# Performance work log

Hardware: AMD Instinct MI355X
Metric: run time of the kernel (lower is better)

The kernel has to match this reference:

```python
import jax, jax.numpy as jnp
import numpy as np

G1 = 8      # channel groups
G2 = 16     # spatial blocks per side
C1, C2 = 128, 64
H1 = W1 = 128
H2 = W2 = 256
BS1 = H1 // G2   # 8  -> 64 elems per x1 block
BS2 = H2 // G2   # 16 -> 256 elems per x2 block
BN_EPS = 1e-5


def setup_inputs() -> dict:
    key = jax.random.key(0)
    ks = jax.random.split(key, 16)
    B = 4
    c1g, c2g = C1 // G1, C2 // G1          # 16, 8
    inp = {
        "x1": jax.random.normal(ks[0], (B, C1, H1, W1), jnp.float32),
        "x2": jax.random.normal(ks[1], (B, C2, H2, W2), jnp.float32),
        # Conv1: conv1d k=1, C1//G1 -> C1//2//G1  (16 -> 8)
        "w_c1": jax.random.normal(ks[2], (c1g // 2, c1g), jnp.float32) * 0.1,
        "b_c1": jnp.zeros((c1g // 2,), jnp.float32),
        # Conv2: conv1d k=1, C2//G1 -> C2//G1  (8 -> 8)
        "w_c2": jax.random.normal(ks[3], (c2g, c2g), jnp.float32) * 0.1,
        "b_c2": jnp.zeros((c2g,), jnp.float32),
        # conv1 / conv2: 1x1 conv2d to 1 channel
        "w_p1": jax.random.normal(ks[4], (C1,), jnp.float32) * 0.1,
        "b_p1": jnp.zeros((), jnp.float32),
        "w_p2": jax.random.normal(ks[5], (C2,), jnp.float32) * 0.1,
        "b_p2": jnp.zeros((), jnp.float32),
        # SpatialAttention linear: 64 -> 256 (torch weight layout [out, in])
        "w_lin": jax.random.normal(ks[6], (BS2 * BS2, BS1 * BS1), jnp.float32) * 0.1,
        "b_lin": jnp.zeros((BS2 * BS2,), jnp.float32),
        # convbnrelu: 1x1 conv C2->C2 + BN (eval mode, running stats mean=0 var=1)
        "w_f": jax.random.normal(ks[7], (C2, C2), jnp.float32) * 0.05,
        "b_f": jnp.zeros((C2,), jnp.float32),
        "bn_gamma": jnp.ones((C2,), jnp.float32),
        "bn_beta": jnp.zeros((C2,), jnp.float32),
    }
    return inp


def reference(x1, x2, w_c1, b_c1, w_c2, b_c2, w_p1, b_p1, w_p2, b_p2,
              w_lin, b_lin, w_f, b_f, bn_gamma, bn_beta):
    B = x1.shape[0]
    c1g, c2g = C1 // G1, C2 // G1

    # ---- grouped channel attention (vectorized over the 8 groups) ----
    gap1 = x1.reshape(B, G1, c1g, H1 * W1).mean(-1)           # [B,g,16]
    gap2 = x2.reshape(B, G1, c2g, H2 * W2).mean(-1)           # [B,g,8]
    mlp1 = jax.nn.relu(jnp.einsum('oc,bgc->bgo', w_c1, gap1) + b_c1)  # [B,g,8]
    mlp2 = jax.nn.relu(jnp.einsum('oc,bgc->bgo', w_c2, gap2) + b_c2)  # [B,g,8]
    sem = jnp.einsum('bgo,bgp->bgop', mlp1, mlp2)             # [B,g,8,8]
    cw_logits = jnp.einsum('bgop,bgp->bgo', sem, mlp2)        # [B,g,8]
    cw = jax.nn.softmax(cw_logits, axis=-1)                   # softmax over channel dim
    sem_x2 = (x2.reshape(B, G1, c2g, H2, W2) * cw[..., None, None]
              ).reshape(B, C2, H2, W2)

    # ---- block-wise spatial attention (vectorized over 16x16 blocks) ----
    nb = G2 * G2
    x1b = x1.reshape(B, C1, G2, BS1, G2, BS1).transpose(0, 2, 4, 1, 3, 5)
    x1b = x1b.reshape(B, nb, C1, BS1, BS1)
    x2b = x2.reshape(B, C2, G2, BS2, G2, BS2).transpose(0, 2, 4, 1, 3, 5)
    x2b = x2b.reshape(B, nb, C2, BS2, BS2)

    pos1 = (jnp.einsum('c,bncij->bnij', w_p1, x1b) + b_p1).reshape(B, nb, BS1 * BS1)
    pos2 = (jnp.einsum('c,bncij->bnij', w_p2, x2b) + b_p2).reshape(B, nb, BS2 * BS2)

    x1t = jnp.einsum('oc,bnc->bno', w_lin, pos1) + b_lin      # [B,nb,256]
    # bmm(x2^T, x1t) is an outer product since both are rank-1 per block
    scores = pos2[..., :, None] * x1t[..., None, :]           # [B,nb,256,256]
    aw = jax.nn.softmax(scores, axis=-1)
    weighted = jnp.einsum('bnq,bnqk->bnk', pos2, aw)          # [B,nb,256]
    # torch.cat(dim=2).view(B,1,H2,W2): raw row-major flatten of block outputs
    spa = weighted.reshape(B, 1, H2, W2)

    # ---- fuse: 1x1 conv + BN(eval) + ReLU ----
    pre = sem_x2 + spa
    conv = jnp.einsum('oc,bchw->bohw', w_f, pre) + b_f[:, None, None]
    bn = conv / jnp.sqrt(jnp.float32(1.0 + BN_EPS)) * bn_gamma[:, None, None] \
         + bn_beta[:, None, None]
    return jax.nn.relu(bn)
```

## Files before the change

### kernel.cpp

```cpp
#include <hip/hip_runtime.h>


#define GAP_OFF  0
#define POS1_OFF 768
#define POS2_OFF 66304

typedef __attribute__((ext_vector_type(8))) short short8;
typedef __attribute__((ext_vector_type(4))) float f32x4;
union U8 { short8 s; unsigned int u[4]; };

__global__ __launch_bounds__(256) void k_fuse(const float* __restrict__ x1,
                                              const float* __restrict__ x2,
                                              const float* __restrict__ w_p1,
                                              const float* __restrict__ b_p1,
                                              const float* __restrict__ w_p2,
                                              const float* __restrict__ b_p2,
                                              float* __restrict__ ws) {
  __shared__ float gbuf[64 * 65];
  __shared__ float pbuf[1024];
  int blk = blockIdx.x, t = threadIdx.x;
  int wv = t >> 6, ln = t & 63;
  if (blk < 256) {
    int b = blk >> 6;
    int px0 = (blk & 63) << 8;
    const float* xb = x1 + ((size_t)b << 21) + px0 + (ln << 2);
    float4 pacc; pacc.x = pacc.y = pacc.z = pacc.w = 0.f;
    {
      float gs[16];
#pragma unroll
      for (int i = 0; i < 16; ++i) {
        int c = (i << 2) + wv;
        float4 v = *(const float4*)(xb + ((size_t)c << 14));
        float wc = w_p1[c];
        pacc.x = fmaf(wc, v.x, pacc.x); pacc.y = fmaf(wc, v.y, pacc.y);
        pacc.z = fmaf(wc, v.z, pacc.z); pacc.w = fmaf(wc, v.w, pacc.w);
        gs[i] = (v.x + v.y) + (v.z + v.w);
      }
#pragma unroll
      for (int i = 0; i < 16; ++i) gbuf[((wv << 4) + i) * 65 + ln] = gs[i];
    }
    __syncthreads();
    if (t < 64) {
      const float* gp = &gbuf[t * 65];
      float s0 = 0.f, s1 = 0.f, s2 = 0.f, s3 = 0.f;
#pragma unroll
      for (int k = 0; k < 64; k += 4) { s0 += gp[k]; s1 += gp[k+1]; s2 += gp[k+2]; s3 += gp[k+3]; }
      atomicAdd(&ws[GAP_OFF + b * 128 + ((t & 15) << 2) + (t >> 4)], (s0 + s1) + (s2 + s3));
    }
    __syncthreads();
    {
      float gs[16];
#pragma unroll
      for (int i = 0; i < 16; ++i) {
        int c = 64 + (i << 2) + wv;
        float4 v = *(const float4*)(xb + ((size_t)c << 14));
        float wc = w_p1[c];
        pacc.x = fmaf(wc, v.x, pacc.x); pacc.y = fmaf(wc, v.y, pacc.y);
        pacc.z = fmaf(wc, v.z, pacc.z); pacc.w = fmaf(wc, v.w, pacc.w);
        gs[i] = (v.x + v.y) + (v.z + v.w);
      }
#pragma unroll
      for (int i = 0; i < 16; ++i) gbuf[((wv << 4) + i) * 65 + ln] = gs[i];
    }
    *(float4*)&pbuf[(wv << 8) + (ln << 2)] = pacc;
    __syncthreads();
    if (t < 64) {
      const float* gp = &gbuf[t * 65];
      float s0 = 0.f, s1 = 0.f, s2 = 0.f, s3 = 0.f;
#pragma unroll
      for (int k = 0; k < 64; k += 4) { s0 += gp[k]; s1 += gp[k+1]; s2 += gp[k+2]; s3 += gp[k+3]; }
      atomicAdd(&ws[GAP_OFF + b * 128 + 64 + ((t & 15) << 2) + (t >> 4)], (s0 + s1) + (s2 + s3));
    }
    float s = (pbuf[t] + pbuf[256 + t]) + (pbuf[512 + t] + pbuf[768 + t]) + b_p1[0];
    int p = px0 + t, h = p >> 7, w0 = p & 127;
    int n = ((h >> 3) << 4) + (w0 >> 3);
    ws[POS1_OFF + ((b * 256 + n) << 6) + ((h & 7) << 3) + (w0 & 7)] = s;
  } else {
    int j = blk - 256;
    int b = j >> 8;
    int row = j & 255;
    const float* xb = x2 + ((size_t)b << 22) + (row << 8) + (ln << 2);
    float4 pacc; pacc.x = pacc.y = pacc.z = pacc.w = 0.f;
    float gs[16];
#pragma unroll
    for (int i = 0; i < 16; ++i) {
      int c = (i << 2) + wv;
      float4 v = *(const float4*)(xb + ((size_t)c << 16));
      float wc = w_p2[c];
      pacc.x = fmaf(wc, v.x, pacc.x); pacc.y = fmaf(wc, v.y, pacc.y);
      pacc.z = fmaf(wc, v.z, pacc.z); pacc.w = fmaf(wc, v.w, pacc.w);
      gs[i] = (v.x + v.y) + (v.z + v.w);
    }
#pragma unroll
    for (int i = 0; i < 16; ++i) gbuf[((wv << 4) + i) * 65 + ln] = gs[i];
    *(float4*)&pbuf[(wv << 8) + (ln << 2)] = pacc;
    __syncthreads();
    if (t < 64) {
      int w2 = t >> 4, i2 = t & 15;
      int c = (i2 << 2) + w2;
      const float* gp = &gbuf[t * 65];
      float s0 = 0.f, s1 = 0.f, s2 = 0.f, s3 = 0.f;
#pragma unroll
      for (int k = 0; k < 64; k += 4) { s0 += gp[k]; s1 += gp[k+1]; s2 += gp[k+2]; s3 += gp[k+3]; }
      atomicAdd(&ws[GAP_OFF + 512 + b * 64 + c], (s0 + s1) + (s2 + s3));
    }
    float s = (pbuf[t] + pbuf[256 + t]) + (pbuf[512 + t] + pbuf[768 + t]) + b_p2[0];
    int n = ((row >> 4) << 4) + (t >> 4);
    ws[POS2_OFF + ((b * 256 + n) << 8) + ((row & 15) << 4) + (t & 15)] = s;
  }
}

__global__ __launch_bounds__(256, 4) void k_mrg(const float* __restrict__ x2,
                                                const float* __restrict__ w_lin,
                                                const float* __restrict__ b_lin,
                                                const float* __restrict__ w_c1,
                                                const float* __restrict__ b_c1,
                                                const float* __restrict__ w_c2,
                                                const float* __restrict__ b_c2,
                                                const float* __restrict__ w_f,
                                                const float* __restrict__ b_f,
                                                const float* __restrict__ gm,
                                                const float* __restrict__ bt,
                                                const float* __restrict__ ws,
                                                float* __restrict__ out) {
  __shared__ unsigned short aHi[4096];
  __shared__ float P1[64], V[256], A2[256], T[256], spa_s[256];
  __shared__ float g1s[128], g2s[64], cw_l[64], p2s[64], p3s[64];
  __shared__ float rmx[4], rmn[4];
  const float L2E = 1.44269504088896f;
  const float kbn = 0.99999500003749969f;
  int t = threadIdx.x;
  int blk = blockIdx.x;
  int b = blk >> 8, n = blk & 255;

  if (t < 128) g1s[t] = ws[GAP_OFF + b * 128 + t] * (1.f / 16384.f);
  if (t < 64)  g2s[t] = ws[GAP_OFF + 512 + b * 64 + t] * (1.f / 65536.f);
  if (t < 64)  P1[t] = ws[POS1_OFF + blk * 64 + t];
  float a = ws[POS2_OFF + blk * 256 + t];
  float a2 = a * L2E;
  A2[t] = a2;
  __syncthreads();

  float v = b_lin[t];
  const float* wr = w_lin + t * 64;
#pragma unroll 16
  for (int c = 0; c < 64; ++c) v = fmaf(wr[c], P1[c], v);
  V[t] = v;
  float vmax = v, vmin = v;
#pragma unroll
  for (int m = 32; m; m >>= 1) {
    vmax = fmaxf(vmax, __shfl_xor(vmax, m));
    vmin = fminf(vmin, __shfl_xor(vmin, m));
  }
  if ((t & 63) == 0) { rmx[t >> 6] = vmax; rmn[t >> 6] = vmin; }
  if (t < 8) {
    int g = t;
    const float* g1 = g1s + g * 16;
    const float* g2 = g2s + g * 8;
    float m1[8];
    for (int o = 0; o < 8; ++o) {
      float s = b_c1[o];
      for (int c = 0; c < 16; ++c) s = fmaf(w_c1[o * 16 + c], g1[c], s);
      m1[o] = fmaxf(s, 0.f);
    }
    float ss = 0.f;
    for (int p = 0; p < 8; ++p) {
      float s = b_c2[p];
      for (int c = 0; c < 8; ++c) s = fmaf(w_c2[p * 8 + c], g2[c], s);
      float r = fmaxf(s, 0.f);
      ss = fmaf(r, r, ss);
    }
    float lg[8], mx = -1e30f;
    for (int o = 0; o < 8; ++o) { lg[o] = m1[o] * ss; mx = fmaxf(mx, lg[o]); }
    float se = 0.f;
    for (int o = 0; o < 8; ++o) {
      lg[o] = __builtin_amdgcn_exp2f((lg[o] - mx) * L2E);
      se += lg[o];
    }
    float inv = 1.f / se;
    for (int o = 0; o < 8; ++o) cw_l[g * 8 + o] = lg[o] * inv;
  }
  __syncthreads();

  vmax = fmaxf(fmaxf(rmx[0], rmx[1]), fmaxf(rmx[2], rmx[3]));
  vmin = fminf(fminf(rmn[0], rmn[1]), fminf(rmn[2], rmn[3]));
  float m2 = (a2 > 0.f) ? a2 * vmax : a2 * vmin;
  float d0 = 0.f, d1 = 0.f, d2 = 0.f, d3 = 0.f;
#pragma unroll 4
  for (int k = 0; k < 256; k += 4) {
    float4 vv = *(float4*)&V[k];
    d0 += __builtin_amdgcn_exp2f(fmaf(a2, vv.x, -m2));
    d1 += __builtin_amdgcn_exp2f(fmaf(a2, vv.y, -m2));
    d2 += __builtin_amdgcn_exp2f(fmaf(a2, vv.z, -m2));
    d3 += __builtin_amdgcn_exp2f(fmaf(a2, vv.w, -m2));
  }
  float den = (d0 + d1) + (d2 + d3);
  T[t] = (a / den) * __builtin_amdgcn_exp2f(-m2);
  if (t < 64) {
    const float4* wrow = (const float4*)(w_f + t * 64);
    float s0 = 0.f, s1 = 0.f, s2 = 0.f, s3 = 0.f;
#pragma unroll
    for (int k = 0; k < 16; ++k) {
      float4 wv = wrow[k];
      s0 += wv.x; s1 += wv.y; s2 += wv.z; s3 += wv.w;
    }
    float A = kbn * gm[t];
    p2s[t] = ((s0 + s1) + (s2 + s3)) * A;
    p3s[t] = fmaf(b_f[t], A, bt[t]);
  }
  __syncthreads();

  float c0 = 0.f, c1 = 0.f, c2 = 0.f, c3 = 0.f;
#pragma unroll 4
  for (int q = 0; q < 256; q += 4) {
    float4 aq = *(float4*)&A2[q];
    float4 tq = *(float4*)&T[q];
    c0 = fmaf(tq.x, __builtin_amdgcn_exp2f(aq.x * v), c0);
    c1 = fmaf(tq.y, __builtin_amdgcn_exp2f(aq.y * v), c1);
    c2 = fmaf(tq.z, __builtin_amdgcn_exp2f(aq.z * v), c2);
    c3 = fmaf(tq.w, __builtin_amdgcn_exp2f(aq.w * v), c3);
  }
  spa_s[t] = (c0 + c1) + (c2 + c3);
  {
    unsigned int* aU = (unsigned int*)aHi;
#pragma unroll
    for (int gi = 0; gi < 4; ++gi) {
      int o = (gi << 4) + ((t >> 2) & 15);
      float ga = kbn * gm[o];
#pragma unroll
      for (int gk = 0; gk < 2; ++gk) {
        int c = (gk << 5) + ((t >> 6) << 3) + ((t & 3) << 1);
        float2 wf2 = *(const float2*)(w_f + (o << 6) + c);
        float v0 = wf2.x * cw_l[c] * ga;
        float v1 = wf2.y * cw_l[c + 1] * ga;
        unsigned int u0 = __float_as_uint(v0), u1 = __float_as_uint(v1);
        unsigned int r0 = (u0 + 0x7FFFu + ((u0 >> 16) & 1u)) >> 16;
        unsigned int r1 = (u1 + 0x7FFFu + ((u1 >> 16) & 1u)) & 0xFFFF0000u;
        aU[(((gi << 1) + gk) << 8) + t] = r0 | r1;
      }
    }
  }
  __syncthreads();

  {
    int l = t & 63;
    int w = t >> 6;
    int pcol = l & 15;
    int krow = l >> 4;
    short8 afr[4][2];
#pragma unroll
    for (int i = 0; i < 4; ++i)
#pragma unroll
      for (int ks = 0; ks < 2; ++ks)
        afr[i][ks] = *(const short8*)&aHi[(((i << 1) + ks) << 9) + (l << 3)];
    float p2v[16], p3v[16];
#pragma unroll
    for (int i = 0; i < 4; ++i)
#pragma unroll
      for (int r = 0; r < 4; ++r) {
        int o = (i << 4) + (krow << 2) + r;
        p2v[(i << 2) + r] = p2s[o];
        p3v[(i << 2) + r] = p3s[o];
      }
    const float* xbase = x2 + ((size_t)b << 22) + (n << 8) + (w << 6) + pcol
                         + ((size_t)(krow << 3) << 16);
    float* obase = out + ((size_t)b << 22) + (n << 8) + (w << 6) + pcol;
    for (int jt = 0; jt < 4; ++jt) {
      const float* xp = xbase + (jt << 4);
      float xv[2][8];
#pragma unroll
      for (int ks = 0; ks < 2; ++ks)
#pragma unroll
        for (int j = 0; j < 8; ++j)
          xv[ks][j] = xp[(size_t)((ks << 5) + j) << 16];
      U8 bh[2], bl[2];
#pragma unroll
      for (int ks = 0; ks < 2; ++ks)
#pragma unroll
        for (int q = 0; q < 4; ++q) {
          float f0 = xv[ks][2 * q], f1 = xv[ks][2 * q + 1];
          unsigned int u0 = __float_as_uint(f0), u1 = __float_as_uint(f1);
          unsigned int h0 = u0 & 0xFFFF0000u, h1 = u1 & 0xFFFF0000u;
          bh[ks].u[q] = (u0 >> 16) | h1;
          float e0 = f0 - __uint_as_float(h0);
          float e1 = f1 - __uint_as_float(h1);
          bl[ks].u[q] = (__float_as_uint(e0) >> 16) | (__float_as_uint(e1) & 0xFFFF0000u);
        }
      f32x4 acc[4] = {};
#pragma unroll
      for (int i = 0; i < 4; ++i) {
#pragma unroll
        for (int ks = 0; ks < 2; ++ks) {
          acc[i] = __builtin_amdgcn_mfma_f32_16x16x32_bf16(afr[i][ks], bh[ks].s, acc[i], 0, 0, 0);
          acc[i] = __builtin_amdgcn_mfma_f32_16x16x32_bf16(afr[i][ks], bl[ks].s, acc[i], 0, 0, 0);
        }
      }
      float spa_p = spa_s[(w << 6) + (jt << 4) + pcol];
#pragma unroll
      for (int i = 0; i < 4; ++i) {
#pragma unroll
        for (int r = 0; r < 4; ++r) {
          int o = (i << 4) + (krow << 2) + r;
          float val = fmaf(spa_p, p2v[(i << 2) + r], acc[i][r] + p3v[(i << 2) + r]);
          obase[(jt << 4) + ((size_t)o << 16)] = fmaxf(val, 0.f);
        }
      }
    }
  }
}

extern "C" void kernel_launch(void* const* d_in, const int* in_sizes, int n_in,
                              void* d_out, int out_size, void* d_ws, size_t ws_size,
                              hipStream_t stream) {
  const float* x1   = (const float*)d_in[0];
  const float* x2   = (const float*)d_in[1];
  const float* w_c1 = (const float*)d_in[2];
  const float* b_c1 = (const float*)d_in[3];
  const float* w_c2 = (const float*)d_in[4];
  const float* b_c2 = (const float*)d_in[5];
  const float* w_p1 = (const float*)d_in[6];
  const float* b_p1 = (const float*)d_in[7];
  const float* w_p2 = (const float*)d_in[8];
  const float* b_p2 = (const float*)d_in[9];
  const float* w_lin= (const float*)d_in[10];
  const float* b_lin= (const float*)d_in[11];
  const float* w_f  = (const float*)d_in[12];
  const float* b_f  = (const float*)d_in[13];
  const float* gmm  = (const float*)d_in[14];
  const float* btt  = (const float*)d_in[15];
  float* ws  = (float*)d_ws;
  float* out = (float*)d_out;

  hipMemsetAsync(ws, 0, 768 * sizeof(float), stream);
  hipLaunchKernelGGL(k_fuse, dim3(1280), dim3(256), 0, stream, x1, x2, w_p1, b_p1, w_p2, b_p2, ws);
  hipLaunchKernelGGL(k_mrg,  dim3(1024), dim3(256), 0, stream, x2, w_lin, b_lin,
                     w_c1, b_c1, w_c2, b_c2, w_f, b_f, gmm, btt, ws, out);
}
```

Measured before the change: 199.2 us.

## Prefetch x2 tile before softmax and drop max-shift in spatial softmax

Result: slower. 210.7 us (+5.8%).

```diff
diff --git a/kernel.cpp b/kernel.cpp
--- a/kernel.cpp
+++ b/kernel.cpp
@@ -25,43 +25,18 @@
     int px0 = (blk & 63) << 8;
     const float* xb = x1 + ((size_t)b << 21) + px0 + (ln << 2);
     float4 pacc; pacc.x = pacc.y = pacc.z = pacc.w = 0.f;
-    {
-      float gs[16];
-#pragma unroll
-      for (int i = 0; i < 16; ++i) {
-        int c = (i << 2) + wv;
-        float4 v = *(const float4*)(xb + ((size_t)c << 14));
-        float wc = w_p1[c];
-        pacc.x = fmaf(wc, v.x, pacc.x); pacc.y = fmaf(wc, v.y, pacc.y);
-        pacc.z = fmaf(wc, v.z, pacc.z); pacc.w = fmaf(wc, v.w, pacc.w);
-        gs[i] = (v.x + v.y) + (v.z + v.w);
-      }
-#pragma unroll
-      for (int i = 0; i < 16; ++i) gbuf[((wv << 4) + i) * 65 + ln] = gs[i];
-    }
-    __syncthreads();
-    if (t < 64) {
-      const float* gp = &gbuf[t * 65];
-      float s0 = 0.f, s1 = 0.f, s2 = 0.f, s3 = 0.f;
-#pragma unroll
-      for (int k = 0; k < 64; k += 4) { s0 += gp[k]; s1 += gp[k+1]; s2 += gp[k+2]; s3 += gp[k+3]; }
-      atomicAdd(&ws[GAP_OFF + b * 128 + ((t & 15) << 2) + (t >> 4)], (s0 + s1) + (s2 + s3));
-    }
-    __syncthreads();
-    {
-      float gs[16];
-#pragma unroll
-      for (int i = 0; i < 16; ++i) {
-        int c = 64 + (i << 2) + wv;
-        float4 v = *(const float4*)(xb + ((size_t)c << 14));
-        float wc = w_p1[c];
-        pacc.x = fmaf(wc, v.x, pacc.x); pacc.y = fmaf(wc, v.y, pacc.y);
-        pacc.z = fmaf(wc, v.z, pacc.z); pacc.w = fmaf(wc, v.w, pacc.w);
-        gs[i] = (v.x + v.y) + (v.z + v.w);
-      }
-#pragma unroll
-      for (int i = 0; i < 16; ++i) gbuf[((wv << 4) + i) * 65 + ln] = gs[i];
-    }
+    float gs[32];
+#pragma unroll
+    for (int i = 0; i < 32; ++i) {
+      int c = (i << 2) + wv;
+      float4 v = *(const float4*)(xb + ((size_t)c << 14));
+      float wc = w_p1[c];
+      pacc.x = fmaf(wc, v.x, pacc.x); pacc.y = fmaf(wc, v.y, pacc.y);
+      pacc.z = fmaf(wc, v.z, pacc.z); pacc.w = fmaf(wc, v.w, pacc.w);
+      gs[i] = (v.x + v.y) + (v.z + v.w);
+    }
+#pragma unroll
+    for (int i = 0; i < 16; ++i) gbuf[((wv << 4) + i) * 65 + ln] = gs[i];
     *(float4*)&pbuf[(wv << 8) + (ln << 2)] = pacc;
     __syncthreads();
     if (t < 64) {
@@ -69,12 +44,23 @@
       float s0 = 0.f, s1 = 0.f, s2 = 0.f, s3 = 0.f;
 #pragma unroll
       for (int k = 0; k < 64; k += 4) { s0 += gp[k]; s1 += gp[k+1]; s2 += gp[k+2]; s3 += gp[k+3]; }
-      atomicAdd(&ws[GAP_OFF + b * 128 + 64 + ((t & 15) << 2) + (t >> 4)], (s0 + s1) + (s2 + s3));
+      atomicAdd(&ws[GAP_OFF + b * 128 + ((t & 15) << 2) + (t >> 4)], (s0 + s1) + (s2 + s3));
     }
     float s = (pbuf[t] + pbuf[256 + t]) + (pbuf[512 + t] + pbuf[768 + t]) + b_p1[0];
     int p = px0 + t, h = p >> 7, w0 = p & 127;
     int n = ((h >> 3) << 4) + (w0 >> 3);
     ws[POS1_OFF + ((b * 256 + n) << 6) + ((h & 7) << 3) + (w0 & 7)] = s;
+    __syncthreads();
+#pragma unroll
+    for (int i = 16; i < 32; ++i) gbuf[((wv << 4) + (i - 16)) * 65 + ln] = gs[i];
+    __syncthreads();
+    if (t < 64) {
+      const float* gp = &gbuf[t * 65];
+      float s0 = 0.f, s1 = 0.f, s2 = 0.f, s3 = 0.f;
+#pragma unroll
+      for (int k = 0; k < 64; k += 4) { s0 += gp[k]; s1 += gp[k+1]; s2 += gp[k+2]; s3 += gp[k+3]; }
+      atomicAdd(&ws[GAP_OFF + b * 128 + 64 + ((t & 15) << 2) + (t >> 4)], (s0 + s1) + (s2 + s3));
+    }
   } else {
     int j = blk - 256;
     int b = j >> 8;
@@ -110,23 +96,22 @@
   }
 }
 
-__global__ __launch_bounds__(256, 4) void k_mrg(const float* __restrict__ x2,
-                                                const float* __restrict__ w_lin,
-                                                const float* __restrict__ b_lin,
-                                                const float* __restrict__ w_c1,
-                                                const float* __restrict__ b_c1,
-                                                const float* __restrict__ w_c2,
-                                                const float* __restrict__ b_c2,
-                                                const float* __restrict__ w_f,
-                                                const float* __restrict__ b_f,
-                                                const float* __restrict__ gm,
-                                                const float* __restrict__ bt,
-                                                const float* __restrict__ ws,
-                                                float* __restrict__ out) {
+__global__ __launch_bounds__(256) void k_mrg(const float* __restrict__ x2,
+                                             const float* __restrict__ w_lin,
+                                             const float* __restrict__ b_lin,
+                                             const float* __restrict__ w_c1,
+                                             const float* __restrict__ b_c1,
+                                             const float* __restrict__ w_c2,
+                                             const float* __restrict__ b_c2,
+                                             const float* __restrict__ w_f,
+                                             const float* __restrict__ b_f,
+                                             const float* __restrict__ gm,
+                                             const float* __restrict__ bt,
+                                             const float* __restrict__ ws,
+                                             float* __restrict__ out) {
   __shared__ unsigned short aHi[4096];
   __shared__ float P1[64], V[256], A2[256], T[256], spa_s[256];
   __shared__ float g1s[128], g2s[64], cw_l[64], p2s[64], p3s[64];
-  __shared__ float rmx[4], rmn[4];
   const float L2E = 1.44269504088896f;
   const float kbn = 0.99999500003749969f;
   int t = threadIdx.x;
@@ -139,20 +124,40 @@
   float a = ws[POS2_OFF + blk * 256 + t];
   float a2 = a * L2E;
   A2[t] = a2;
+  if (t < 64) {
+    const float4* wrow = (const float4*)(w_f + t * 64);
+    float s0 = 0.f, s1 = 0.f, s2 = 0.f, s3 = 0.f;
+#pragma unroll
+    for (int k = 0; k < 16; ++k) {
+      float4 wv = wrow[k];
+      s0 += wv.x; s1 += wv.y; s2 += wv.z; s3 += wv.w;
+    }
+    float A = kbn * gm[t];
+    p2s[t] = ((s0 + s1) + (s2 + s3)) * A;
+    p3s[t] = fmaf(b_f[t], A, bt[t]);
+  }
   __syncthreads();
+
+  int l = t & 63;
+  int wq = t >> 6;
+  int pcol = l & 15;
+  int krow = l >> 4;
+  const float* xbase = x2 + ((size_t)b << 22) + (n << 8) + (wq << 6) + pcol
+                       + ((size_t)(krow << 3) << 16);
+  float xv[4][2][8];
+#pragma unroll
+  for (int jt = 0; jt < 4; ++jt)
+#pragma unroll
+    for (int ks = 0; ks < 2; ++ks)
+#pragma unroll
+      for (int j = 0; j < 8; ++j)
+        xv[jt][ks][j] = xbase[(jt << 4) + ((size_t)((ks << 5) + j) << 16)];
 
   float v = b_lin[t];
   const float* wr = w_lin + t * 64;
 #pragma unroll 16
   for (int c = 0; c < 64; ++c) v = fmaf(wr[c], P1[c], v);
   V[t] = v;
-  float vmax = v, vmin = v;
-#pragma unroll
-  for (int m = 32; m; m >>= 1) {
-    vmax = fmaxf(vmax, __shfl_xor(vmax, m));
-    vmin = fminf(vmin, __shfl_xor(vmin, m));
-  }
-  if ((t & 63) == 0) { rmx[t >> 6] = vmax; rmn[t >> 6] = vmin; }
   if (t < 8) {
     int g = t;
     const float* g1 = g1s + g * 16;
@@ -180,47 +185,23 @@
     float inv = 1.f / se;
     for (int o = 0; o < 8; ++o) cw_l[g * 8 + o] = lg[o] * inv;
   }
+  U8 bh[4][2], bl[4][2];
+#pragma unroll
+  for (int jt = 0; jt < 4; ++jt)
+#pragma unroll
+    for (int ks = 0; ks < 2; ++ks)
+#pragma unroll
+      for (int q = 0; q < 4; ++q) {
+        float f0 = xv[jt][ks][2 * q], f1 = xv[jt][ks][2 * q + 1];
+        unsigned int u0 = __float_as_uint(f0), u1 = __float_as_uint(f1);
+        unsigned int h0 = u0 & 0xFFFF0000u, h1 = u1 & 0xFFFF0000u;
+        bh[jt][ks].u[q] = (u0 >> 16) | h1;
+        float e0 = f0 - __uint_as_float(h0);
+        float e1 = f1 - __uint_as_float(h1);
+        bl[jt][ks].u[q] = (__float_as_uint(e0) >> 16) | (__float_as_uint(e1) & 0xFFFF0000u);
+      }
   __syncthreads();
 
-  vmax = fmaxf(fmaxf(rmx[0], rmx[1]), fmaxf(rmx[2], rmx[3]));
-  vmin = fminf(fminf(rmn[0], rmn[1]), fminf(rmn[2], rmn[3]));
-  float m2 = (a2 > 0.f) ? a2 * vmax : a2 * vmin;
-  float d0 = 0.f, d1 = 0.f, d2 = 0.f, d3 = 0.f;
-#pragma unroll 4
-  for (int k = 0; k < 256; k += 4) {
-    float4 vv = *(float4*)&V[k];
-    d0 += __builtin_amdgcn_exp2f(fmaf(a2, vv.x, -m2));
-    d1 += __builtin_amdgcn_exp2f(fmaf(a2, vv.y, -m2));
-    d2 += __builtin_amdgcn_exp2f(fmaf(a2, vv.z, -m2));
-    d3 += __builtin_amdgcn_exp2f(fmaf(a2, vv.w, -m2));
-  }
-  float den = (d0 + d1) + (d2 + d3);
-  T[t] = (a / den) * __builtin_amdgcn_exp2f(-m2);
-  if (t < 64) {
-    const float4* wrow = (const float4*)(w_f + t * 64);
-    float s0 = 0.f, s1 = 0.f, s2 = 0.f, s3 = 0.f;
-#pragma unroll
-    for (int k = 0; k < 16; ++k) {
-      float4 wv = wrow[k];
-      s0 += wv.x; s1 += wv.y; s2 += wv.z; s3 += wv.w;
-    }
-    float A = kbn * gm[t];
-    p2s[t] = ((s0 + s1) + (s2 + s3)) * A;
-    p3s[t] = fmaf(b_f[t], A, bt[t]);
-  }
-  __syncthreads();
-
-  float c0 = 0.f, c1 = 0.f, c2 = 0.f, c3 = 0.f;
-#pragma unroll 4
-  for (int q = 0; q < 256; q += 4) {
-    float4 aq = *(float4*)&A2[q];
-    float4 tq = *(float4*)&T[q];
-    c0 = fmaf(tq.x, __builtin_amdgcn_exp2f(aq.x * v), c0);
-    c1 = fmaf(tq.y, __builtin_amdgcn_exp2f(aq.y * v), c1);
-    c2 = fmaf(tq.z, __builtin_amdgcn_exp2f(aq.z * v), c2);
-    c3 = fmaf(tq.w, __builtin_amdgcn_exp2f(aq.w * v), c3);
-  }
-  spa_s[t] = (c0 + c1) + (c2 + c3);
   {
     unsigned int* aU = (unsigned int*)aHi;
 #pragma unroll
@@ -240,70 +221,55 @@
       }
     }
   }
+  float d0 = 0.f, d1 = 0.f, d2 = 0.f, d3 = 0.f;
+#pragma unroll 4
+  for (int k = 0; k < 256; k += 4) {
+    float4 vv = *(float4*)&V[k];
+    d0 += __builtin_amdgcn_exp2f(a2 * vv.x);
+    d1 += __builtin_amdgcn_exp2f(a2 * vv.y);
+    d2 += __builtin_amdgcn_exp2f(a2 * vv.z);
+    d3 += __builtin_amdgcn_exp2f(a2 * vv.w);
+  }
+  float den = (d0 + d1) + (d2 + d3);
+  T[t] = a / den;
   __syncthreads();
 
-  {
-    int l = t & 63;
-    int w = t >> 6;
-    int pcol = l & 15;
-    int krow = l >> 4;
-    short8 afr[4][2];
-#pragma unroll
-    for (int i = 0; i < 4; ++i)
-#pragma unroll
-      for (int ks = 0; ks < 2; ++ks)
-        afr[i][ks] = *(const short8*)&aHi[(((i << 1) + ks) << 9) + (l << 3)];
-    float p2v[16], p3v[16];
-#pragma unroll
-    for (int i = 0; i < 4; ++i)
+  short8 afr[4][2];
+#pragma unroll
+  for (int i = 0; i < 4; ++i)
+#pragma unroll
+    for (int ks = 0; ks < 2; ++ks)
+      afr[i][ks] = *(const short8*)&aHi[(((i << 1) + ks) << 9) + (l << 3)];
+  float c0 = 0.f, c1 = 0.f, c2 = 0.f, c3 = 0.f;
+#pragma unroll 4
+  for (int q = 0; q < 256; q += 4) {
+    float4 aq = *(float4*)&A2[q];
+    float4 tq = *(float4*)&T[q];
+    c0 = fmaf(tq.x, __builtin_amdgcn_exp2f(aq.x * v), c0);
+    c1 = fmaf(tq.y, __builtin_amdgcn_exp2f(aq.y * v), c1);
+    c2 = fmaf(tq.z, __builtin_amdgcn_exp2f(aq.z * v), c2);
+    c3 = fmaf(tq.w, __builtin_amdgcn_exp2f(aq.w * v), c3);
+  }
+  spa_s[t] = (c0 + c1) + (c2 + c3);
+  __syncthreads();
+
+  float* obase = out + ((size_t)b << 22) + (n << 8) + (wq << 6) + pcol;
+#pragma unroll
+  for (int jt = 0; jt < 4; ++jt) {
+    float spa_p = spa_s[(wq << 6) + (jt << 4) + pcol];
+#pragma unroll
+    for (int i = 0; i < 4; ++i) {
+      f32x4 acc = {};
+#pragma unroll
+      for (int ks = 0; ks < 2; ++ks) {
+        acc = __builtin_amdgcn_mfma_f32_16x16x32_bf16(afr[i][ks], bh[jt][ks].s, acc, 0, 0, 0);
+        acc = __builtin_amdgcn_mfma_f32_16x16x32_bf16(afr[i][ks], bl[jt][ks].s, acc, 0, 0, 0);
+      }
 #pragma unroll
       for (int r = 0; r < 4; ++r) {
         int o = (i << 4) + (krow << 2) + r;
-        p2v[(i << 2) + r] = p2s[o];
-        p3v[(i << 2) + r] = p3s[o];
-      }
-    const float* xbase = x2 + ((size_t)b << 22) + (n << 8) + (w << 6) + pcol
-                         + ((size_t)(krow << 3) << 16);
-    float* obase = out + ((size_t)b << 22) + (n << 8) + (w << 6) + pcol;
-    for (int jt = 0; jt < 4; ++jt) {
-      const float* xp = xbase + (jt << 4);
-      float xv[2][8];
-#pragma unroll
-      for (int ks = 0; ks < 2; ++ks)
-#pragma unroll
-        for (int j = 0; j < 8; ++j)
-          xv[ks][j] = xp[(size_t)((ks << 5) + j) << 16];
-      U8 bh[2], bl[2];
-#pragma unroll
-      for (int ks = 0; ks < 2; ++ks)
-#pragma unroll
-        for (int q = 0; q < 4; ++q) {
-          float f0 = xv[ks][2 * q], f1 = xv[ks][2 * q + 1];
-          unsigned int u0 = __float_as_uint(f0), u1 = __float_as_uint(f1);
-          unsigned int h0 = u0 & 0xFFFF0000u, h1 = u1 & 0xFFFF0000u;
-          bh[ks].u[q] = (u0 >> 16) | h1;
-          float e0 = f0 - __uint_as_float(h0);
-          float e1 = f1 - __uint_as_float(h1);
-          bl[ks].u[q] = (__float_as_uint(e0) >> 16) | (__float_as_uint(e1) & 0xFFFF0000u);
-        }
-      f32x4 acc[4] = {};
-#pragma unroll
-      for (int i = 0; i < 4; ++i) {
-#pragma unroll
-        for (int ks = 0; ks < 2; ++ks) {
-          acc[i] = __builtin_amdgcn_mfma_f32_16x16x32_bf16(afr[i][ks], bh[ks].s, acc[i], 0, 0, 0);
-          acc[i] = __builtin_amdgcn_mfma_f32_16x16x32_bf16(afr[i][ks], bl[ks].s, acc[i], 0, 0, 0);
-        }
-      }
-      float spa_p = spa_s[(w << 6) + (jt << 4) + pcol];
-#pragma unroll
-      for (int i = 0; i < 4; ++i) {
-#pragma unroll
-        for (int r = 0; r < 4; ++r) {
-          int o = (i << 4) + (krow << 2) + r;
-          float val = fmaf(spa_p, p2v[(i << 2) + r], acc[i][r] + p3v[(i << 2) + r]);
-          obase[(jt << 4) + ((size_t)o << 16)] = fmaxf(val, 0.f);
-        }
+        float val = fmaf(spa_p, p2s[o], acc[r] + p3s[o]);
+        obase[(jt << 4) + ((size_t)o << 16)] = fmaxf(val, 0.f);
       }
     }
   }
```
